# Performance work log

Measured on AMD Instinct MI355X. Metric: run time of the kernel, lower is better.

Reference implementation:

```python
import jax, jax.numpy as jnp
import numpy as np

IN_FEATURES = 4096
OUT_FEATURES = 11008
PACK_COLS = IN_FEATURES // 2
BATCH, SEQ = 2, 2048


def setup_inputs() -> dict:
    key = jax.random.key(0)
    k_x, k_w, k_s, k_b = jax.random.split(key, 4)
    x = jax.random.normal(k_x, (BATCH, SEQ, IN_FEATURES), dtype=jnp.float32)
    # packed uint8 values (two int4 nibbles per byte), stored as int32 in [0, 256)
    weight_packed = jax.random.randint(k_w, (OUT_FEATURES, PACK_COLS), 0, 256, dtype=jnp.int32)
    # per-output-row dequant scale (abs_max/7 in the original); small positive values
    scale = jax.random.uniform(k_s, (OUT_FEATURES,), dtype=jnp.float32, minval=0.001, maxval=0.02)
    bias = jax.random.normal(k_b, (OUT_FEATURES,), dtype=jnp.float32)
    return {"x": x, "weight_packed": weight_packed, "scale": scale, "bias": bias}


def _dequantize(weight_packed, scale):
    # low nibble stored first (even columns), high nibble second (odd columns)
    lo = (weight_packed & 15) - 8          # [out, pack_cols] int32 in [-8, 7]
    hi = ((weight_packed >> 4) & 15) - 8   # [out, pack_cols]
    # interleave lo/hi -> [out, 2*pack_cols] matching w[:, 0::2]=lo, w[:, 1::2]=hi
    w_int = jnp.stack([lo, hi], axis=-1).reshape(OUT_FEATURES, 2 * PACK_COLS)
    w_int = w_int[:, :IN_FEATURES]
    return w_int.astype(jnp.float32) * scale[:, None]  # [out, in] fp32


def reference(x, weight_packed, scale, bias):
    w = _dequantize(weight_packed, scale)                 # [out, in]
    # F.linear: x @ w.T + bias
    return jnp.einsum('bsi,oi->bso', x, w) + bias
```

## Files before the change

kernel.cpp:

```cpp
#include <hip/hip_runtime.h>
#include <hip/hip_fp16.h>

#define M_TOTAL 4096
#define N_TOTAL 11008
#define K_TOTAL 4096
#define KPACK   2048

typedef _Float16 f16x4 __attribute__((ext_vector_type(4)));
typedef _Float16 f16x8 __attribute__((ext_vector_type(8)));
typedef float    f32x4 __attribute__((ext_vector_type(4)));

__device__ __forceinline__ void load16_to_lds(const void* g, void* l) {
    __builtin_amdgcn_global_load_lds(
        (const __attribute__((address_space(1))) unsigned int*)g,
        (__attribute__((address_space(3))) unsigned int*)l,
        16, 0, 0);
}

__global__ __launch_bounds__(256)
void _Int4Linear_cvt_x(const float* __restrict__ x, _Float16* __restrict__ xf) {
    const size_t i = ((size_t)blockIdx.x * 256 + threadIdx.x) * 8;
    const float4 v0 = *(const float4*)(x + i);
    const float4 v1 = *(const float4*)(x + i + 4);
    f16x8 h = { (_Float16)v0.x, (_Float16)v0.y, (_Float16)v0.z, (_Float16)v0.w,
                (_Float16)v1.x, (_Float16)v1.y, (_Float16)v1.z, (_Float16)v1.w };
    *(f16x8*)(xf + i) = h;
}

__global__ __launch_bounds__(256)
void _Int4Linear_dequant_w(const int* __restrict__ wp, _Float16* __restrict__ wf) {
    const size_t i = ((size_t)blockIdx.x * 256 + threadIdx.x) * 4;
    const int4 p = *(const int4*)(wp + i);
    const int v[4] = { p.x, p.y, p.z, p.w };
    f16x8 h;
    #pragma unroll
    for (int j = 0; j < 4; ++j) {
        h[2 * j]     = (_Float16)(( v[j]       & 15) - 8);
        h[2 * j + 1] = (_Float16)(((v[j] >> 4) & 15) - 8);
    }
    *(f16x8*)(wf + i * 2) = h;
}

#define BM 256
#define BN 256
#define NKT 64

__global__ __launch_bounds__(512, 2)
void _Int4Linear_54631984005366_kernel(const _Float16* __restrict__ A,
                                       const _Float16* __restrict__ B,
                                       const float* __restrict__ scale,
                                       const float* __restrict__ bias,
                                       float*       __restrict__ out)
{
    extern __shared__ char sm[];
    char* const smA = sm;
    char* const smB = sm + 65536;

    const int t    = threadIdx.x;
    const int wave = t >> 6;
    const int lane = t & 63;
    const int l16  = lane & 15;
    const int quad = lane >> 4;
    const int wm   = wave >> 2;
    const int wn   = wave & 3;

    const int b0 = blockIdx.x;
    const int sw = (b0 & 7) * 86 + (b0 >> 3);
    const int mBase = (sw & 15) * BM;
    const int nBase = (sw >> 4) * BN;

    const int srow = wave * 16 + (lane >> 2);
    const int scol = (((lane & 3) ^ ((lane >> 3) & 3)) << 3);
    const _Float16* const Ab = A + (size_t)(mBase + srow) * K_TOTAL + scol;
    const _Float16* const Bb = B + (size_t)(nBase + srow) * K_TOTAL + scol;
    const int ldst = wave * 1024;

    const int chA  = (quad ^ ((l16 >> 1) & 3)) << 4;
    const int aoff = (wm * 128 + l16) * 64 + chA;
    const int boff = (wn * 64  + l16) * 64 + chA;

    f32x4 acc[8][4] = {};

    #pragma unroll
    for (int r = 0; r < 2; ++r) load16_to_lds(Ab + (size_t)r * 128 * K_TOTAL,      smA + r * 8192 + ldst);
    #pragma unroll
    for (int r = 0; r < 2; ++r) load16_to_lds(Bb + (size_t)r * 128 * K_TOTAL,      smB + r * 8192 + ldst);
    #pragma unroll
    for (int r = 0; r < 2; ++r) load16_to_lds(Ab + (size_t)r * 128 * K_TOTAL + 32, smA + 16384 + r * 8192 + ldst);
    #pragma unroll
    for (int r = 0; r < 2; ++r) load16_to_lds(Bb + (size_t)r * 128 * K_TOTAL + 32, smB + 16384 + r * 8192 + ldst);
    asm volatile("s_waitcnt vmcnt(4)" ::: "memory");
    __builtin_amdgcn_s_barrier();
    asm volatile("" ::: "memory");

    #pragma unroll 2
    for (int t0 = 0; t0 < NKT; ++t0) {
        const int par = (t0 & 1) * 2;
        const int nxp = ((t0 + 1) & 1) * 2;
        const int tn  = (t0 < NKT - 1) ? (t0 + 1) : t0;
        const int kn  = tn * 64;
        char* const Ac0 = smA + (par    ) * 16384;
        char* const Ac1 = smA + (par + 1) * 16384;
        char* const Bc0 = smB + (par    ) * 16384;
        char* const Bc1 = smB + (par + 1) * 16384;
        char* const An0 = smA + (nxp    ) * 16384;
        char* const An1 = smA + (nxp + 1) * 16384;
        char* const Bn0 = smB + (nxp    ) * 16384;
        char* const Bn1 = smB + (nxp + 1) * 16384;

        f16x8 a[4], b[4];

        #pragma unroll
        for (int f = 0; f < 4; ++f) a[f] = *(const f16x8*)(Ac0 + aoff + f * 1024);
        #pragma unroll
        for (int f = 0; f < 4; ++f) b[f] = *(const f16x8*)(Bc0 + boff + f * 1024);
        #pragma unroll
        for (int r = 0; r < 2; ++r) load16_to_lds(Ab + (size_t)r * 128 * K_TOTAL + kn, An0 + r * 8192 + ldst);
        __builtin_amdgcn_s_barrier();
        asm volatile("s_waitcnt lgkmcnt(0)" ::: "memory");
        __builtin_amdgcn_sched_barrier(0);
        __builtin_amdgcn_s_setprio(1);
        #pragma unroll
        for (int mf = 0; mf < 4; ++mf)
            #pragma unroll
            for (int nf = 0; nf < 4; ++nf)
                acc[mf][nf] = __builtin_amdgcn_mfma_f32_16x16x32_f16(a[mf], b[nf], acc[mf][nf], 0, 0, 0);
        __builtin_amdgcn_s_setprio(0);
        __builtin_amdgcn_s_barrier();
        asm volatile("" ::: "memory");

        #pragma unroll
        for (int f = 0; f < 4; ++f) a[f] = *(const f16x8*)(Ac0 + aoff + 4096 + f * 1024);
        #pragma unroll
        for (int r = 0; r < 2; ++r) load16_to_lds(Bb + (size_t)r * 128 * K_TOTAL + kn, Bn0 + r * 8192 + ldst);
        __builtin_amdgcn_s_barrier();
        asm volatile("s_waitcnt lgkmcnt(0)" ::: "memory");
        __builtin_amdgcn_sched_barrier(0);
        __builtin_amdgcn_s_setprio(1);
        #pragma unroll
        for (int mf = 0; mf < 4; ++mf)
            #pragma unroll
            for (int nf = 0; nf < 4; ++nf)
                acc[4 + mf][nf] = __builtin_amdgcn_mfma_f32_16x16x32_f16(a[mf], b[nf], acc[4 + mf][nf], 0, 0, 0);
        __builtin_amdgcn_s_setprio(0);
        asm volatile("s_waitcnt vmcnt(4)" ::: "memory");
        __builtin_amdgcn_s_barrier();
        asm volatile("" ::: "memory");

        #pragma unroll
        for (int f = 0; f < 4; ++f) a[f] = *(const f16x8*)(Ac1 + aoff + f * 1024);
        #pragma unroll
        for (int f = 0; f < 4; ++f) b[f] = *(const f16x8*)(Bc1 + boff + f * 1024);
        #pragma unroll
        for (int r = 0; r < 2; ++r) load16_to_lds(Ab + (size_t)r * 128 * K_TOTAL + kn + 32, An1 + r * 8192 + ldst);
        __builtin_amdgcn_s_barrier();
        asm volatile("s_waitcnt lgkmcnt(0)" ::: "memory");
        __builtin_amdgcn_sched_barrier(0);
        __builtin_amdgcn_s_setprio(1);
        #pragma unroll
        for (int mf = 0; mf < 4; ++mf)
            #pragma unroll
            for (int nf = 0; nf < 4; ++nf)
                acc[mf][nf] = __builtin_amdgcn_mfma_f32_16x16x32_f16(a[mf], b[nf], acc[mf][nf], 0, 0, 0);
        __builtin_amdgcn_s_setprio(0);
        __builtin_amdgcn_s_barrier();
        asm volatile("" ::: "memory");

        #pragma unroll
        for (int f = 0; f < 4; ++f) a[f] = *(const f16x8*)(Ac1 + aoff + 4096 + f * 1024);
        #pragma unroll
        for (int r = 0; r < 2; ++r) load16_to_lds(Bb + (size_t)r * 128 * K_TOTAL + kn + 32, Bn1 + r * 8192 + ldst);
        __builtin_amdgcn_s_barrier();
        asm volatile("s_waitcnt lgkmcnt(0)" ::: "memory");
        __builtin_amdgcn_sched_barrier(0);
        __builtin_amdgcn_s_setprio(1);
        #pragma unroll
        for (int mf = 0; mf < 4; ++mf)
            #pragma unroll
            for (int nf = 0; nf < 4; ++nf)
                acc[4 + mf][nf] = __builtin_amdgcn_mfma_f32_16x16x32_f16(a[mf], b[nf], acc[4 + mf][nf], 0, 0, 0);
        __builtin_amdgcn_s_setprio(0);
        asm volatile("s_waitcnt vmcnt(4)" ::: "memory");
        __builtin_amdgcn_s_barrier();
        asm volatile("" ::: "memory");
    }
    asm volatile("s_waitcnt vmcnt(0)" ::: "memory");

    #pragma unroll
    for (int nf = 0; nf < 4; ++nf) {
        const int n = nBase + wn * 64 + nf * 16 + l16;
        const float s  = scale[n];
        const float bz = bias[n];
        #pragma unroll
        for (int mf = 0; mf < 8; ++mf) {
            const int mb = mBase + wm * 128 + mf * 16 + quad * 4;
            #pragma unroll
            for (int r = 0; r < 4; ++r)
                out[(size_t)(mb + r) * N_TOTAL + n] = acc[mf][nf][r] * s + bz;
        }
    }
}

#define FBM 128
#define FBN 128
#define FBK 32
#define LDR 40
__global__ __launch_bounds__(256)
void _Int4Linear_fallback(const float* __restrict__ x, const int* __restrict__ wp,
                          const float* __restrict__ scale, const float* __restrict__ bias,
                          float* __restrict__ out)
{
    __shared__ _Float16 As[FBM * LDR];
    __shared__ _Float16 Bs[FBN * LDR];
    const int t = threadIdx.x, wave = t >> 6, lane = t & 63;
    const int l16 = lane & 15, quad = lane >> 4;
    const int nBase = blockIdx.x * FBN, mBase = blockIdx.y * FBM;
    const int wm = (wave >> 1) * 64, wn = (wave & 1) * 64;
    f32x4 acc[4][4] = {};
    for (int k0 = 0; k0 < K_TOTAL; k0 += FBK) {
        #pragma unroll
        for (int i = 0; i < 4; ++i) {
            const int li = i * 256 + t, row = li >> 3, c4 = li & 7;
            const float4 v = *(const float4*)(&x[(size_t)(mBase + row) * K_TOTAL + k0 + c4 * 4]);
            f16x4 hv = { (_Float16)v.x, (_Float16)v.y, (_Float16)v.z, (_Float16)v.w };
            *(f16x4*)(&As[row * LDR + c4 * 4]) = hv;
        }
        #pragma unroll
        for (int i = 0; i < 2; ++i) {
            const int li = i * 256 + t, row = li >> 2, c4 = li & 3;
            const int4 p = *(const int4*)(&wp[(size_t)(nBase + row) * KPACK + (k0 >> 1) + c4 * 4]);
            const int vals[4] = { p.x, p.y, p.z, p.w };
            f16x8 hv;
            #pragma unroll
            for (int j = 0; j < 4; ++j) {
                hv[2 * j]     = (_Float16)(( vals[j]       & 15) - 8);
                hv[2 * j + 1] = (_Float16)(((vals[j] >> 4) & 15) - 8);
            }
            *(f16x8*)(&Bs[row * LDR + c4 * 8]) = hv;
        }
        __syncthreads();
        f16x8 a[4], b[4];
        #pragma unroll
        for (int mt = 0; mt < 4; ++mt)
            a[mt] = *(const f16x8*)(&As[(wm + mt * 16 + l16) * LDR + quad * 8]);
        #pragma unroll
        for (int nt = 0; nt < 4; ++nt)
            b[nt] = *(const f16x8*)(&Bs[(wn + nt * 16 + l16) * LDR + quad * 8]);
        #pragma unroll
        for (int mt = 0; mt < 4; ++mt)
            #pragma unroll
            for (int nt = 0; nt < 4; ++nt)
                acc[mt][nt] = __builtin_amdgcn_mfma_f32_16x16x32_f16(a[mt], b[nt], acc[mt][nt], 0, 0, 0);
        __syncthreads();
    }
    #pragma unroll
    for (int nt = 0; nt < 4; ++nt) {
        const int n = nBase + wn + nt * 16 + l16;
        const float s = scale[n], bz = bias[n];
        #pragma unroll
        for (int mt = 0; mt < 4; ++mt)
            #pragma unroll
            for (int r = 0; r < 4; ++r)
                out[(size_t)(mBase + wm + mt * 16 + quad * 4 + r) * N_TOTAL + n] = acc[mt][nt][r] * s + bz;
    }
}

extern "C" void kernel_launch(void* const* d_in, const int* in_sizes, int n_in,
                              void* d_out, int out_size, void* d_ws, size_t ws_size,
                              hipStream_t stream) {
    const float* x     = (const float*)d_in[0];
    const int*   wp    = (const int*)d_in[1];
    const float* scale = (const float*)d_in[2];
    const float* bias  = (const float*)d_in[3];
    float*       out   = (float*)d_out;

    const size_t xf_bytes = (size_t)M_TOTAL * K_TOTAL * 2;
    const size_t wf_bytes = (size_t)N_TOTAL * K_TOTAL * 2;

    static int lds_attr_state = 0;
    if (lds_attr_state == 0) {
        hipError_t e = hipFuncSetAttribute(
            (const void*)_Int4Linear_54631984005366_kernel,
            hipFuncAttributeMaxDynamicSharedMemorySize, 131072);
        lds_attr_state = (e == hipSuccess) ? 1 : -1;
    }

    if (ws_size >= xf_bytes + wf_bytes && lds_attr_state == 1) {
        _Float16* xf = (_Float16*)d_ws;
        _Float16* wf = (_Float16*)((char*)d_ws + xf_bytes);
        _Int4Linear_cvt_x<<<8192, 256, 0, stream>>>(x, xf);
        _Int4Linear_dequant_w<<<22016, 256, 0, stream>>>(wp, wf);
        _Int4Linear_54631984005366_kernel<<<dim3(688), dim3(512), 131072, stream>>>(xf, wf, scale, bias, out);
    } else {
        dim3 grid(N_TOTAL / FBN, M_TOTAL / FBM);
        _Int4Linear_fallback<<<grid, 256, 0, stream>>>(x, wp, scale, bias, out);
    }
}
```

Before: 631.1 us.

## Merge per-half MFMA phases into one phase per k-substep, cutting barriers

The main loop goes from four barrier-separated phases per iteration, each loading half the A fragments and running 16 MFMAs, to two phases. Each new phase issues both A and B global-to-LDS prefetches up front, reads all 8 A and 4 B fragments from LDS, then runs 32 MFMAs. This removes half the workgroup barriers and explicit lgkmcnt waits and lets the compiler overlap LDS reads with MFMAs. In exchange it uses more registers for operands, which may reduce occupancy, and the LDS read latency is no longer hidden by the barrier interleaving.

```diff
diff --git a/kernel.cpp b/kernel.cpp
--- a/kernel.cpp
+++ b/kernel.cpp
@@ -91,7 +91,7 @@
     for (int r = 0; r < 2; ++r) load16_to_lds(Bb + (size_t)r * 128 * K_TOTAL + 32, smB + 16384 + r * 8192 + ldst);
     asm volatile("s_waitcnt vmcnt(4)" ::: "memory");
     __builtin_amdgcn_s_barrier();
-    asm volatile("" ::: "memory");
+    __builtin_amdgcn_sched_barrier(0);
 
     #pragma unroll 2
     for (int t0 = 0; t0 < NKT; ++t0) {
@@ -108,81 +108,49 @@
         char* const Bn0 = smB + (nxp    ) * 16384;
         char* const Bn1 = smB + (nxp + 1) * 16384;
 
-        f16x8 a[4], b[4];
-
-        #pragma unroll
-        for (int f = 0; f < 4; ++f) a[f] = *(const f16x8*)(Ac0 + aoff + f * 1024);
-        #pragma unroll
-        for (int f = 0; f < 4; ++f) b[f] = *(const f16x8*)(Bc0 + boff + f * 1024);
-        #pragma unroll
-        for (int r = 0; r < 2; ++r) load16_to_lds(Ab + (size_t)r * 128 * K_TOTAL + kn, An0 + r * 8192 + ldst);
-        __builtin_amdgcn_s_barrier();
-        asm volatile("s_waitcnt lgkmcnt(0)" ::: "memory");
-        __builtin_amdgcn_sched_barrier(0);
-        __builtin_amdgcn_s_setprio(1);
-        #pragma unroll
-        for (int mf = 0; mf < 4; ++mf)
-            #pragma unroll
-            for (int nf = 0; nf < 4; ++nf)
-                acc[mf][nf] = __builtin_amdgcn_mfma_f32_16x16x32_f16(a[mf], b[nf], acc[mf][nf], 0, 0, 0);
-        __builtin_amdgcn_s_setprio(0);
-        __builtin_amdgcn_s_barrier();
-        asm volatile("" ::: "memory");
-
-        #pragma unroll
-        for (int f = 0; f < 4; ++f) a[f] = *(const f16x8*)(Ac0 + aoff + 4096 + f * 1024);
-        #pragma unroll
-        for (int r = 0; r < 2; ++r) load16_to_lds(Bb + (size_t)r * 128 * K_TOTAL + kn, Bn0 + r * 8192 + ldst);
-        __builtin_amdgcn_s_barrier();
-        asm volatile("s_waitcnt lgkmcnt(0)" ::: "memory");
-        __builtin_amdgcn_sched_barrier(0);
-        __builtin_amdgcn_s_setprio(1);
-        #pragma unroll
-        for (int mf = 0; mf < 4; ++mf)
-            #pragma unroll
-            for (int nf = 0; nf < 4; ++nf)
-                acc[4 + mf][nf] = __builtin_amdgcn_mfma_f32_16x16x32_f16(a[mf], b[nf], acc[4 + mf][nf], 0, 0, 0);
-        __builtin_amdgcn_s_setprio(0);
-        asm volatile("s_waitcnt vmcnt(4)" ::: "memory");
-        __builtin_amdgcn_s_barrier();
-        asm volatile("" ::: "memory");
-
-        #pragma unroll
-        for (int f = 0; f < 4; ++f) a[f] = *(const f16x8*)(Ac1 + aoff + f * 1024);
-        #pragma unroll
-        for (int f = 0; f < 4; ++f) b[f] = *(const f16x8*)(Bc1 + boff + f * 1024);
-        #pragma unroll
-        for (int r = 0; r < 2; ++r) load16_to_lds(Ab + (size_t)r * 128 * K_TOTAL + kn + 32, An1 + r * 8192 + ldst);
-        __builtin_amdgcn_s_barrier();
-        asm volatile("s_waitcnt lgkmcnt(0)" ::: "memory");
-        __builtin_amdgcn_sched_barrier(0);
-        __builtin_amdgcn_s_setprio(1);
-        #pragma unroll
-        for (int mf = 0; mf < 4; ++mf)
-            #pragma unroll
-            for (int nf = 0; nf < 4; ++nf)
-                acc[mf][nf] = __builtin_amdgcn_mfma_f32_16x16x32_f16(a[mf], b[nf], acc[mf][nf], 0, 0, 0);
-        __builtin_amdgcn_s_setprio(0);
-        __builtin_amdgcn_s_barrier();
-        asm volatile("" ::: "memory");
-
-        #pragma unroll
-        for (int f = 0; f < 4; ++f) a[f] = *(const f16x8*)(Ac1 + aoff + 4096 + f * 1024);
-        #pragma unroll
-        for (int r = 0; r < 2; ++r) load16_to_lds(Bb + (size_t)r * 128 * K_TOTAL + kn + 32, Bn1 + r * 8192 + ldst);
-        __builtin_amdgcn_s_barrier();
-        asm volatile("s_waitcnt lgkmcnt(0)" ::: "memory");
-        __builtin_amdgcn_sched_barrier(0);
-        __builtin_amdgcn_s_setprio(1);
-        #pragma unroll
-        for (int mf = 0; mf < 4; ++mf)
-            #pragma unroll
-            for (int nf = 0; nf < 4; ++nf)
-                acc[4 + mf][nf] = __builtin_amdgcn_mfma_f32_16x16x32_f16(a[mf], b[nf], acc[4 + mf][nf], 0, 0, 0);
-        __builtin_amdgcn_s_setprio(0);
-        asm volatile("s_waitcnt vmcnt(4)" ::: "memory");
-        __builtin_amdgcn_s_barrier();
-        asm volatile("" ::: "memory");
+        {
+            #pragma unroll
+            for (int r = 0; r < 2; ++r) load16_to_lds(Ab + (size_t)r * 128 * K_TOTAL + kn, An0 + r * 8192 + ldst);
+            #pragma unroll
+            for (int r = 0; r < 2; ++r) load16_to_lds(Bb + (size_t)r * 128 * K_TOTAL + kn, Bn0 + r * 8192 + ldst);
+            f16x8 a[8], b[4];
+            #pragma unroll
+            for (int f = 0; f < 8; ++f) a[f] = *(const f16x8*)(Ac0 + aoff + f * 1024);
+            #pragma unroll
+            for (int f = 0; f < 4; ++f) b[f] = *(const f16x8*)(Bc0 + boff + f * 1024);
+            __builtin_amdgcn_s_setprio(1);
+            #pragma unroll
+            for (int mf = 0; mf < 8; ++mf)
+                #pragma unroll
+                for (int nf = 0; nf < 4; ++nf)
+                    acc[mf][nf] = __builtin_amdgcn_mfma_f32_16x16x32_f16(a[mf], b[nf], acc[mf][nf], 0, 0, 0);
+            __builtin_amdgcn_s_setprio(0);
+            asm volatile("s_waitcnt vmcnt(4)" ::: "memory");
+            __builtin_amdgcn_s_barrier();
+            __builtin_amdgcn_sched_barrier(0);
+        }
+
+        {
+            #pragma unroll
+            for (int r = 0; r < 2; ++r) load16_to_lds(Ab + (size_t)r * 128 * K_TOTAL + kn + 32, An1 + r * 8192 + ldst);
+            #pragma unroll
+            for (int r = 0; r < 2; ++r) load16_to_lds(Bb + (size_t)r * 128 * K_TOTAL + kn + 32, Bn1 + r * 8192 + ldst);
+            f16x8 a[8], b[4];
+            #pragma unroll
+            for (int f = 0; f < 8; ++f) a[f] = *(const f16x8*)(Ac1 + aoff + f * 1024);
+            #pragma unroll
+            for (int f = 0; f < 4; ++f) b[f] = *(const f16x8*)(Bc1 + boff + f * 1024);
+            __builtin_amdgcn_s_setprio(1);
+            #pragma unroll
+            for (int mf = 0; mf < 8; ++mf)
+                #pragma unroll
+                for (int nf = 0; nf < 4; ++nf)
+                    acc[mf][nf] = __builtin_amdgcn_mfma_f32_16x16x32_f16(a[mf], b[nf], acc[mf][nf], 0, 0, 0);
+            __builtin_amdgcn_s_setprio(0);
+            asm volatile("s_waitcnt vmcnt(4)" ::: "memory");
+            __builtin_amdgcn_s_barrier();
+            __builtin_amdgcn_sched_barrier(0);
+        }
     }
     asm volatile("s_waitcnt vmcnt(0)" ::: "memory");
 
```

Result: no change. 620.7 us (-1.6%).
